# Performance work log

Hardware: AMD Instinct MI355X
Metric: run time of the kernel (lower is better)

Reference implementation:

```python
import jax, jax.numpy as jnp
import numpy as np

B, T, C, H = 4, 1024, 512, 4
D = C // H
N_LAYER, LAYER_ID = 12, 1


def setup_inputs() -> dict:
    key = jax.random.key(0)
    ks = jax.random.split(key, 10)
    w = lambda k, shape: 0.02 * jax.random.normal(k, shape, dtype=jnp.float32)

    r01 = LAYER_ID / (N_LAYER - 1)          # ratio_0_to_1
    r1a0 = 1.0 - LAYER_ID / N_LAYER          # ratio_1_to_almost0
    i = np.arange(C, dtype=np.float32)
    time_decay = (-5.0 + 8.0 * (i / (C - 1)) ** (0.7 + 1.3 * r01)).astype(np.float32)
    xv = i / C
    tm_q = (xv ** r1a0).astype(np.float32)[None, None, :]
    tm_k = (xv ** r1a0).astype(np.float32)[None, None, :]
    tm_v = ((xv ** r1a0) + 0.3 * r01).astype(np.float32)[None, None, :]
    tm_g = (xv ** (0.5 * r1a0)).astype(np.float32)[None, None, :]

    return dict(
        x=jax.random.normal(ks[0], (B, T, C), dtype=jnp.float32),
        ln1_g=jnp.ones((C,), jnp.float32), ln1_b=jnp.zeros((C,), jnp.float32),
        ln2_g=jnp.ones((C,), jnp.float32), ln2_b=jnp.zeros((C,), jnp.float32),
        time_decay=jnp.asarray(time_decay),
        tm_q=jnp.asarray(tm_q), tm_k=jnp.asarray(tm_k),
        tm_v=jnp.asarray(tm_v), tm_g=jnp.asarray(tm_g),
        Wq=w(ks[1], (C, C)), Wk=w(ks[2], (C, C)), Wv=w(ks[3], (C, C)),
        Wg=w(ks[4], (C, C)), Wo=w(ks[5], (C, C)),
        rms_scale=jnp.ones((C,), jnp.float32),
        W1=w(ks[6], (4 * C, C)), W2=w(ks[7], (C, 4 * C)),
    )


def layernorm(x, g, b, eps=1e-5):
    m = x.mean(-1, keepdims=True)
    v = ((x - m) ** 2).mean(-1, keepdims=True)
    return g * (x - m) / jnp.sqrt(v + eps) + b


def rmsnorm(x, scale, eps=1e-8):
    # matches: norm = ||x||_2 / sqrt(dim); out = scale * x / (norm + eps)
    norm = jnp.sqrt(jnp.sum(x * x, axis=-1, keepdims=True)) / (x.shape[-1] ** 0.5)
    return scale * (x / (norm + eps))


def lnssm_scan(q, k, v, lam):
    """Decayed linear-attention scan. q,k,v: [B,T,H,D]; lam: [H,D] (decay over k index).
    Returns S: [B,T,H,D] = q_t^T A_t, Zs: [B,T,H] = q_t . z_t."""
    qT, kT, vT = (jnp.moveaxis(a, 1, 0) for a in (q, k, v))  # [T,B,H,D]
    Bq = q.shape[0]
    A0 = jnp.zeros((Bq, q.shape[2], q.shape[3], q.shape[3]), q.dtype)
    z0 = jnp.zeros((Bq, q.shape[2], q.shape[3]), q.dtype)

    def step(carry, inp):
        A, z = carry
        qt, kt, vt = inp
        A = lam[None, :, :, None] * A + kt[..., None] * vt[..., None, :]  # [B,H,Dk,Dv]
        z = lam[None] * z + kt                                            # [B,H,Dk]
        St = jnp.einsum('bhi,bhij->bhj', qt, A)
        Zt = jnp.einsum('bhi,bhi->bh', qt, z)
        return (A, z), (St, Zt)

    _, (S, Zs) = jax.lax.scan(step, (A0, z0), (qT, kT, vT))
    return jnp.moveaxis(S, 0, 1), jnp.moveaxis(Zs, 0, 1)


def reference(x, ln1_g, ln1_b, ln2_g, ln2_b, time_decay, tm_q, tm_k, tm_v, tm_g,
              Wq, Wk, Wv, Wg, Wo, rms_scale, W1, W2):
    Bx, Tx, Cx = x.shape
    Hh, Dd = H, Cx // H

    # --- TimeMix on ln1(x) ---
    h = layernorm(x, ln1_g, ln1_b)
    xx = jnp.concatenate([jnp.zeros_like(h[:, :1]), h[:, :-1]], axis=1)  # time shift
    xq = h * tm_q + xx * (1 - tm_q)
    xk = h * tm_k + xx * (1 - tm_k)
    xv_ = h * tm_v + xx * (1 - tm_v)
    xg = h * tm_g + xx * (1 - tm_g)
    q = xq @ Wq.T
    k = xk @ Wk.T
    v = xv_ @ Wv.T
    g = jax.nn.sigmoid(xg @ Wg.T)
    q = jnp.exp(rmsnorm(q, rms_scale))
    k = jnp.exp(rmsnorm(k, rms_scale))

    lam = jnp.exp(-jnp.exp(time_decay)).reshape(Hh, Dd)
    qh = q.reshape(Bx, Tx, Hh, Dd)
    kh = k.reshape(Bx, Tx, Hh, Dd)
    vh = v.reshape(Bx, Tx, Hh, Dd)
    S, Zs = lnssm_scan(qh, kh, vh, lam)
    att = (S / Zs[..., None]).reshape(Bx, Tx, Cx)
    att = (g * att) @ Wo.T
    x = x + att

    # --- ChannelMix on ln2(x) ---
    h2 = layernorm(x, ln2_g, ln2_b)
    x = x + jax.nn.gelu(h2 @ W1.T, approximate=False) @ W2.T
    return x
```

## Files before the change

kernel.cpp:

```cpp
#include <hip/hip_runtime.h>
#include <math.h>

#define Bb 4
#define Tt 1024
#define Cc 512
#define Hh 4
#define Dd 128
#define Mrows (Bb*Tt)
#define NC 32
#define CL 32
#define AUGB_CB 18432

typedef unsigned short u16;
typedef __attribute__((ext_vector_type(8))) short bf16x8;
typedef __attribute__((ext_vector_type(4))) float f32x4;

__device__ __forceinline__ u16 f2bf(float f) {
  unsigned u = __float_as_uint(f);
  unsigned r = (u + 0x7fffu + ((u >> 16) & 1u)) >> 16;
  return (u16)r;
}
__device__ __forceinline__ float bf2f(u16 v) {
  return __uint_as_float((unsigned)v << 16);
}
__device__ __forceinline__ unsigned pack2(float a, float b) {
  return (unsigned)f2bf(a) | ((unsigned)f2bf(b) << 16);
}
__device__ __forceinline__ float rms_r(const float* __restrict__ ssqp, int zsel, int row) {
  const float* p = ssqp + (size_t)zsel*4*Mrows + row;
  float s2 = p[0] + p[Mrows] + p[2*Mrows] + p[3*Mrows];
  float norm = sqrtf(s2) * 0.044194173824159216f;
  return 1.f / (norm + 1e-8f);
}

__global__ __launch_bounds__(256) void ln1mix_kernel(const float* __restrict__ x,
    const float* __restrict__ g, const float* __restrict__ bta,
    const float* __restrict__ tmq, const float* __restrict__ tmk,
    const float* __restrict__ tmv, const float* __restrict__ tmg,
    u16* __restrict__ xqb, u16* __restrict__ xkb,
    u16* __restrict__ xvb, u16* __restrict__ xgb)
{
  int m = blockIdx.x, tid = threadIdx.x;
  const float* xr = x + (size_t)m * Cc;
  float v0 = xr[tid], v1 = xr[tid + 256];
  bool has = (m & (Tt-1)) != 0;
  float u0 = 0.f, u1 = 0.f;
  if (has) { u0 = xr[tid - Cc]; u1 = xr[(int)tid + 256 - Cc]; }
  float sa = v0 + v1, qa = v0*v0 + v1*v1;
  float sb = u0 + u1, qb = u0*u0 + u1*u1;
  #pragma unroll
  for (int off = 32; off > 0; off >>= 1) {
    sa += __shfl_down(sa, off, 64); qa += __shfl_down(qa, off, 64);
    sb += __shfl_down(sb, off, 64); qb += __shfl_down(qb, off, 64);
  }
  __shared__ float r4[4][4];
  int w = tid >> 6;
  if ((tid & 63) == 0) { r4[w][0]=sa; r4[w][1]=qa; r4[w][2]=sb; r4[w][3]=qb; }
  __syncthreads();
  float Sa = r4[0][0]+r4[1][0]+r4[2][0]+r4[3][0];
  float Qa = r4[0][1]+r4[1][1]+r4[2][1]+r4[3][1];
  float Sb = r4[0][2]+r4[1][2]+r4[2][2]+r4[3][2];
  float Qb = r4[0][3]+r4[1][3]+r4[2][3]+r4[3][3];
  float ma = Sa*(1.f/Cc), va = Qa*(1.f/Cc) - ma*ma, ia = rsqrtf(va + 1e-5f);
  float mb = Sb*(1.f/Cc), vb = Qb*(1.f/Cc) - mb*mb, ib = rsqrtf(vb + 1e-5f);
  #pragma unroll
  for (int half = 0; half < 2; ++half) {
    int c = tid + half*256;
    float v = half ? v1 : v0, u = half ? u1 : u0;
    float hv = g[c]*(v - ma)*ia + bta[c];
    float pv = has ? (g[c]*(u - mb)*ib + bta[c]) : 0.f;
    size_t off = ((size_t)(c >> 3) * Mrows + m) * 8 + (c & 7);
    float tq = tmq[c], tk = tmk[c], tv = tmv[c], tg = tmg[c];
    xqb[off] = f2bf(hv*tq + pv*(1.f-tq));
    xkb[off] = f2bf(hv*tk + pv*(1.f-tk));
    xvb[off] = f2bf(hv*tv + pv*(1.f-tv));
    xgb[off] = f2bf(hv*tg + pv*(1.f-tg));
  }
}

__global__ __launch_bounds__(256) void ln2b_kernel(const float* __restrict__ x,
    const float* __restrict__ p0, const float* __restrict__ p1,
    const float* __restrict__ g, const float* __restrict__ bta,
    float* __restrict__ x1, u16* __restrict__ out)
{
  int row = blockIdx.x, tid = threadIdx.x;
  size_t r0 = (size_t)row * Cc + tid, r1 = r0 + 256;
  float v0 = x[r0] + p0[r0] + p1[r0];
  float v1 = x[r1] + p0[r1] + p1[r1];
  x1[r0] = v0; x1[r1] = v1;
  float s = v0 + v1, s2 = v0*v0 + v1*v1;
  #pragma unroll
  for (int off = 32; off > 0; off >>= 1) {
    s  += __shfl_down(s,  off, 64);
    s2 += __shfl_down(s2, off, 64);
  }
  __shared__ float rs[4], rq[4];
  int w = tid >> 6;
  if ((tid & 63) == 0) { rs[w] = s; rq[w] = s2; }
  __syncthreads();
  float S  = rs[0]+rs[1]+rs[2]+rs[3];
  float S2 = rq[0]+rq[1]+rq[2]+rq[3];
  float mean = S * (1.0f/Cc);
  float var  = S2 * (1.0f/Cc) - mean*mean;
  float inv = rsqrtf(var + 1e-5f);
  int c0 = tid, c1 = tid + 256;
  float o0 = g[c0] * (v0-mean)*inv + bta[c0];
  float o1 = g[c1] * (v1-mean)*inv + bta[c1];
  out[((size_t)(c0 >> 3) * Mrows + row) * 8 + (c0 & 7)] = f2bf(o0);
  out[((size_t)(c1 >> 3) * Mrows + row) * 8 + (c1 & 7)] = f2bf(o1);
}

__global__ __launch_bounds__(256) void wconv_all_kernel(
    const float* __restrict__ Wq, const float* __restrict__ Wk,
    const float* __restrict__ Wv, const float* __restrict__ Wg,
    const float* __restrict__ Wo, const float* __restrict__ W1,
    const float* __restrict__ W2, u16* __restrict__ out)
{
  int blk = blockIdx.x;
  const float* src; u16* dst; int K, nshift;
  if (blk < 640) {
    int wsel = blk >> 7;
    src = wsel==0?Wq:wsel==1?Wk:wsel==2?Wv:wsel==3?Wg:Wo;
    dst = out + (size_t)wsel*262144; K = 512; nshift = 9; blk &= 127;
  } else if (blk < 1152) {
    src = W1; dst = out + (size_t)5*262144; K = 512; nshift = 11; blk -= 640;
  } else {
    src = W2; dst = out + (size_t)5*262144 + 1048576; K = 2048; nshift = 9; blk -= 1152;
  }
  int i = blk*256 + threadIdx.x;
  int n = i & ((1 << nshift) - 1), kg = i >> nshift;
  const float* p = src + (size_t)n * K + kg * 8;
  float4 a = *(const float4*)p, b = *(const float4*)(p + 4);
  uint4 o;
  o.x = pack2(a.x, a.y); o.y = pack2(a.z, a.w);
  o.z = pack2(b.x, b.y); o.w = pack2(b.z, b.w);
  *(uint4*)(dst + (size_t)i * 8) = o;
}

template<int MR, int NR, int KR>
__device__ __forceinline__ void gemm_core(const u16* __restrict__ A,
    const u16* __restrict__ W, const float* __restrict__ res,
    float* __restrict__ outf, u16* __restrict__ outb, int act,
    int m0, int n0, u16* Asm, u16* Bsm, float* __restrict__ ssq)
{
  const int tid = threadIdx.x, w = tid >> 6, l = tid & 63;
  const int wr = w >> 1, wc = w & 1;
  f32x4 acc[4][4];
  #pragma unroll
  for (int i = 0; i < 4; ++i)
    #pragma unroll
    for (int j = 0; j < 4; ++j) acc[i][j] = (f32x4){0.f,0.f,0.f,0.f};
  const int kgl = l >> 4, rl = l & 15;
  const int q = w * 4;

  #define STAGE(KT, BUF) do {                                               \
    _Pragma("unroll")                                                       \
    for (int ii = 0; ii < 4; ++ii) {                                        \
      int qq = q + ii;                                                      \
      int isB = qq >> 3, idx = qq & 7, kg = idx >> 1, hf = idx & 1;         \
      const u16* src = isB                                                  \
        ? W + ((size_t)((KT)*4 + kg) * NR + n0 + hf*64 + l) * 8             \
        : A + ((size_t)((KT)*4 + kg) * MR + m0 + hf*64 + l) * 8;            \
      u16* dst = (isB ? Bsm : Asm) + (BUF)*4096 + (kg * 128 + hf * 64) * 8; \
      __builtin_amdgcn_global_load_lds(                                     \
          (const __attribute__((address_space(1))) void*)src,               \
          (__attribute__((address_space(3))) void*)dst, 16, 0, 0);          \
    }                                                                       \
  } while (0)

  constexpr int nk = KR >> 5;
  STAGE(0, 0); STAGE(1, 1);
  int cur = 0;
  for (int kt = 0; kt < nk; ++kt) {
    if (kt == nk - 1) asm volatile("s_waitcnt vmcnt(0)" ::: "memory");
    else              asm volatile("s_waitcnt vmcnt(4)" ::: "memory");
    __builtin_amdgcn_s_barrier();
    bf16x8 af[4], bfr[4];
    #pragma unroll
    for (int f = 0; f < 4; ++f)
      af[f] = *(const bf16x8*)&Asm[cur*4096 + (kgl*128 + wr*64 + f*16 + rl) * 8];
    #pragma unroll
    for (int f = 0; f < 4; ++f)
      bfr[f] = *(const bf16x8*)&Bsm[cur*4096 + (kgl*128 + wc*64 + f*16 + rl) * 8];
    if (kt + 2 < nk) {
      int nb = cur + 2; if (nb >= 3) nb -= 3;
      STAGE(kt + 2, nb);
    }
    __builtin_amdgcn_s_setprio(1);
    #pragma unroll
    for (int i = 0; i < 4; ++i)
      #pragma unroll
      for (int j = 0; j < 4; ++j)
        acc[i][j] = __builtin_amdgcn_mfma_f32_16x16x32_bf16(af[i], bfr[j], acc[i][j], 0, 0, 0);
    __builtin_amdgcn_s_setprio(0);
    if (++cur == 3) cur = 0;
  }
  #undef STAGE

  const int rbase = (l >> 4) * 4, cn = l & 15;
  #pragma unroll
  for (int i = 0; i < 4; ++i) {
    #pragma unroll
    for (int j = 0; j < 4; ++j) {
      #pragma unroll
      for (int r = 0; r < 4; ++r) {
        int m = m0 + wr*64 + i*16 + rbase + r;
        int n = n0 + wc*64 + j*16 + cn;
        float vv = acc[i][j][r];
        if (res) vv += res[(size_t)m * NR + n];
        if (act == 1) vv = 0.5f*vv*(1.f + erff(vv * 0.70710678118f));
        else if (act == 2) vv = 1.f/(1.f + expf(-vv));
        if (outb) outb[((size_t)(n >> 3) * MR + m) * 8 + (n & 7)] = f2bf(vv);
        else outf[(size_t)m * NR + n] = vv;
      }
    }
  }

  if (ssq) {
    __syncthreads();
    float* red2 = (float*)Asm;
    #pragma unroll
    for (int i = 0; i < 4; ++i) {
      #pragma unroll
      for (int r = 0; r < 4; ++r) {
        int row_local = wr*64 + i*16 + rbase + r;
        float sq = 0.f;
        #pragma unroll
        for (int j = 0; j < 4; ++j) { float t = acc[i][j][r]; sq += t*t; }
        red2[row_local*32 + wc*16 + cn] = sq;
      }
    }
    __syncthreads();
    if (tid < 128) {
      float ssum = 0.f;
      #pragma unroll
      for (int u2 = 0; u2 < 32; ++u2) ssum += red2[tid*32 + u2];
      ssq[m0 + tid] = ssum;
    }
  }
}

__global__ __launch_bounds__(256) void gemm_qkvg(const u16* __restrict__ xall,
    const u16* __restrict__ Wall, float* __restrict__ outall, float* __restrict__ ssqp)
{
  __shared__ __align__(16) u16 Asm[3*4096];
  __shared__ __align__(16) u16 Bsm[3*4096];
  int z = blockIdx.z;
  const size_t E = (size_t)Mrows * Cc;
  float* ssq = (z < 2) ? ssqp + ((size_t)z*4 + blockIdx.x)*Mrows : nullptr;
  gemm_core<Mrows,512,512>(xall + z*E, Wall + (size_t)z*262144, nullptr,
            outall + z*E, nullptr, z == 3 ? 2 : 0,
            blockIdx.y * 128, blockIdx.x * 128, Asm, Bsm, ssq);
}

__global__ __launch_bounds__(256) void gemm_wo(const u16* __restrict__ A,
    const u16* __restrict__ W, float* __restrict__ pbuf)
{
  __shared__ __align__(16) u16 Asm[3*4096];
  __shared__ __align__(16) u16 Bsm[3*4096];
  int z = blockIdx.z;
  const size_t E = (size_t)Mrows * Cc;
  gemm_core<Mrows,512,256>(A + (size_t)z*32*Mrows*8, W + (size_t)z*32*512*8, nullptr,
            pbuf + z*E, nullptr, 0, blockIdx.y * 128, blockIdx.x * 128, Asm, Bsm, nullptr);
}

__global__ __launch_bounds__(256) void gemm_w1(const u16* __restrict__ A,
    const u16* __restrict__ W, u16* __restrict__ outb)
{
  __shared__ __align__(16) u16 Asm[3*4096];
  __shared__ __align__(16) u16 Bsm[3*4096];
  gemm_core<Mrows,2048,512>(A, W, nullptr, nullptr, outb, 1,
            blockIdx.y * 128, blockIdx.x * 128, Asm, Bsm, nullptr);
}

__global__ __launch_bounds__(256) void gemm_w2(const u16* __restrict__ A,
    const u16* __restrict__ W, float* __restrict__ pbuf)
{
  __shared__ __align__(16) u16 Asm[3*4096];
  __shared__ __align__(16) u16 Bsm[3*4096];
  int z = blockIdx.z;
  const size_t E = (size_t)Mrows * Cc;
  gemm_core<Mrows,512,512>(A + (size_t)z*64*Mrows*8, W + (size_t)z*64*512*8, nullptr,
            pbuf + z*E, nullptr, 0, blockIdx.y * 128, blockIdx.x * 128, Asm, Bsm, nullptr);
}

__global__ __launch_bounds__(256) void reduce4_kernel(const float* __restrict__ x1,
    const float* __restrict__ p, float* __restrict__ out)
{
  const size_t E = (size_t)Mrows * Cc;
  size_t f = ((size_t)blockIdx.x * 256 + threadIdx.x) * 4;
  float4 a = *(const float4*)(x1 + f);
  float4 q0 = *(const float4*)(p + f);
  float4 q1 = *(const float4*)(p + E + f);
  float4 q2 = *(const float4*)(p + 2*E + f);
  float4 q3 = *(const float4*)(p + 3*E + f);
  float4 o;
  o.x = a.x + q0.x + q1.x + q2.x + q3.x;
  o.y = a.y + q0.y + q1.y + q2.y + q3.y;
  o.z = a.z + q0.z + q1.z + q2.z + q3.z;
  o.w = a.w + q0.w + q1.w + q2.w + q3.w;
  *(float4*)(out + f) = o;
}

__global__ __launch_bounds__(256) void chunk_state_kernel(const float* __restrict__ k,
    const float* __restrict__ v, const float* __restrict__ td,
    const float* __restrict__ rsc, const float* __restrict__ ssqp,
    u16* __restrict__ Augl)
{
  __shared__ float k_lds[CL][Dd];
  __shared__ float v_lds[CL][Dd];
  int blk = blockIdx.x; int c = blk & (NC-1); int bh = blk >> 5;
  int b = bh >> 2, h = bh & 3;
  int tid = threadIdx.x;
  size_t base = ((size_t)b*Tt + (size_t)c*CL)*Cc + h*Dd;
  #pragma unroll
  for (int r = 0; r < 4; ++r) {
    int idx4 = r*256 + tid;
    int s = idx4 >> 5; int i4 = (idx4 & 31) << 2;
    float rk = rms_r(ssqp, 1, b*Tt + c*CL + s);
    float4 kr = *(const float4*)&k[base + (size_t)s*Cc + i4];
    k_lds[s][i4+0] = expf(rsc[h*Dd+i4+0] * kr.x * rk);
    k_lds[s][i4+1] = expf(rsc[h*Dd+i4+1] * kr.y * rk);
    k_lds[s][i4+2] = expf(rsc[h*Dd+i4+2] * kr.z * rk);
    k_lds[s][i4+3] = expf(rsc[h*Dd+i4+3] * kr.w * rk);
    *(float4*)&v_lds[s][i4] = *(const float4*)&v[base + (size_t)s*Cc + i4];
  }
  __syncthreads();
  int iq = tid >> 3; int i0 = iq << 2;
  int jg = tid & 7;  int j0 = jg << 4;
  float lam4[4], powv[4], zacc[4];
  #pragma unroll
  for (int ci=0; ci<4; ++ci) {
    lam4[ci] = expf(-expf(td[h*Dd + i0 + ci]));
    powv[ci] = 1.f; zacc[ci] = 0.f;
  }
  float acc[4][16];
  #pragma unroll
  for (int ci=0; ci<4; ++ci)
    #pragma unroll
    for (int jj=0; jj<16; ++jj) acc[ci][jj] = 0.f;

  for (int s = CL-1; s >= 0; --s) {
    float4 k4 = *(const float4*)&k_lds[s][i0];
    float kw0 = powv[0]*k4.x, kw1 = powv[1]*k4.y, kw2 = powv[2]*k4.z, kw3 = powv[3]*k4.w;
    zacc[0]+=kw0; zacc[1]+=kw1; zacc[2]+=kw2; zacc[3]+=kw3;
    #pragma unroll
    for (int q4 = 0; q4 < 4; ++q4) {
      float4 v4 = *(const float4*)&v_lds[s][j0 + q4*4];
      float vv[4] = {v4.x, v4.y, v4.z, v4.w};
      #pragma unroll
      for (int u=0; u<4; ++u) {
        acc[0][q4*4+u] += kw0*vv[u];
        acc[1][q4*4+u] += kw1*vv[u];
        acc[2][q4*4+u] += kw2*vv[u];
        acc[3][q4*4+u] += kw3*vv[u];
      }
    }
    powv[0]*=lam4[0]; powv[1]*=lam4[1]; powv[2]*=lam4[2]; powv[3]*=lam4[3];
  }
  u16* aug = Augl + ((size_t)c*16 + bh)*AUGB_CB;
  const int ig = i0 >> 3, isub = i0 & 7;
  #pragma unroll
  for (int jj=0; jj<16; ++jj) {
    int j = j0 + jj;
    uint2 pk;
    pk.x = pack2(acc[0][jj], acc[1][jj]);
    pk.y = pack2(acc[2][jj], acc[3][jj]);
    *(uint2*)&aug[(size_t)ig*1152 + (size_t)j*8 + isub] = pk;
  }
  if (jg == 0) {
    uint2 pk;
    pk.x = pack2(zacc[0], zacc[1]);
    pk.y = pack2(zacc[2], zacc[3]);
    *(uint2*)&aug[(size_t)ig*1152 + 128*8 + isub] = pk;
  }
}

__global__ __launch_bounds__(256) void combine_kernel(const u16* __restrict__ Augl,
    const float* __restrict__ td, u16* __restrict__ Augb)
{
  int idx = blockIdx.x*256 + threadIdx.x;
  if (idx >= 129*128) return;
  int bh = blockIdx.y; int h = bh & 3;
  int j = idx >> 7, i = idx & 127;
  size_t aoff = (size_t)(i >> 3) * 1152 + (size_t)j * 8 + (i & 7);
  float lamL = expf(-expf(td[h*Dd + i]) * (float)CL);
  const u16* pl = Augl + (size_t)bh*AUGB_CB + aoff;
  u16* pi = Augb + (size_t)bh*AUGB_CB + aoff;
  float prev = 0.f;
  const size_t cstr = (size_t)16*AUGB_CB;
  for (int c = 0; c < NC; ++c) {
    float val = bf2f(pl[c*cstr]);
    pi[c*cstr] = f2bf(prev);
    prev = lamL*prev + val;
  }
}

__global__ __launch_bounds__(256, 2) void scan_mfma_kernel(
    const float* __restrict__ q, const float* __restrict__ k,
    const float* __restrict__ v, const float* __restrict__ td,
    const float* __restrict__ rsc, const float* __restrict__ ssqp,
    const u16* __restrict__ Augb, const float* __restrict__ gmat,
    u16* __restrict__ out)
{
  __shared__ float k_lds[32*192];
  __shared__ u16  qfrag[32*128];
  __shared__ u16  vfrag[4*1152];
  __shared__ float P32[32*33];
  __shared__ u16  pfrag[32*32];
  __shared__ float lam_lds[128];
  __shared__ float zbuf[32];

  const int tid = threadIdx.x;
  const int blk = blockIdx.x; const int c = blk & 31, bh = blk >> 5;
  const int b = bh >> 2, h = bh & 3;
  const int w = tid >> 6, l = tid & 63;
  const int t = (w << 3) + (l >> 3);
  const int is = l & 7;

  if (tid < 128) lam_lds[tid] = expf(-expf(td[h*Dd + tid]));

  const int grow = b*Tt + c*CL + t;
  const size_t rowbase = ((size_t)grow)*Cc + h*Dd + is*16;
  const float rq = rms_r(ssqp, 0, grow);
  const float rk = rms_r(ssqp, 1, grow);

  float qv[16];
  {
    #pragma unroll
    for (int c4 = 0; c4 < 4; ++c4) {
      float4 q4 = *(const float4*)(q + rowbase + c4*4);
      int e0 = c4*4;
      qv[e0+0] = expf(rsc[h*Dd+is*16+e0+0] * q4.x * rq);
      qv[e0+1] = expf(rsc[h*Dd+is*16+e0+1] * q4.y * rq);
      qv[e0+2] = expf(rsc[h*Dd+is*16+e0+2] * q4.z * rq);
      qv[e0+3] = expf(rsc[h*Dd+is*16+e0+3] * q4.w * rq);
    }
    float lt = (float)(t + 1);
    u16 qt[16];
    #pragma unroll
    for (int e = 0; e < 16; ++e) {
      float el2 = -expf(td[h*Dd + is*16 + e]) * 1.4426950408889634f;
      qt[e] = f2bf(qv[e] * exp2f(el2 * lt));
    }
    #pragma unroll
    for (int hf = 0; hf < 2; ++hf) {
      int k8 = is*2 + hf;
      uint4 pk;
      pk.x = (unsigned)qt[hf*8+0] | ((unsigned)qt[hf*8+1]<<16);
      pk.y = (unsigned)qt[hf*8+2] | ((unsigned)qt[hf*8+3]<<16);
      pk.z = (unsigned)qt[hf*8+4] | ((unsigned)qt[hf*8+5]<<16);
      pk.w = (unsigned)qt[hf*8+6] | ((unsigned)qt[hf*8+7]<<16);
      *(uint4*)&qfrag[t*128 + ((k8 ^ (t&7))<<3)] = pk;
    }
  }
  #pragma unroll
  for (int c4 = 0; c4 < 4; ++c4) {
    float4 k4 = *(const float4*)(k + rowbase + c4*4);
    int e0 = is*16 + c4*4;
    k_lds[t*192 + is*24 + c4*4+0] = expf(rsc[h*Dd+e0+0] * k4.x * rk);
    k_lds[t*192 + is*24 + c4*4+1] = expf(rsc[h*Dd+e0+1] * k4.y * rk);
    k_lds[t*192 + is*24 + c4*4+2] = expf(rsc[h*Dd+e0+2] * k4.z * rk);
    k_lds[t*192 + is*24 + c4*4+3] = expf(rsc[h*Dd+e0+3] * k4.w * rk);
  }
  #pragma unroll
  for (int c4 = 0; c4 < 4; ++c4) {
    float4 v4 = *(const float4*)(v + rowbase + c4*4);
    int j0 = is*16 + c4*4;
    vfrag[(t>>3)*1152 + (j0+0)*8 + (t&7)] = f2bf(v4.x);
    vfrag[(t>>3)*1152 + (j0+1)*8 + (t&7)] = f2bf(v4.y);
    vfrag[(t>>3)*1152 + (j0+2)*8 + (t&7)] = f2bf(v4.z);
    vfrag[(t>>3)*1152 + (j0+3)*8 + (t&7)] = f2bf(v4.w);
  }
  if (tid < 32) vfrag[(tid>>3)*1152 + 128*8 + (tid&7)] = 0x3F80;
  if (tid < 240) {
    #pragma unroll
    for (int u = 0; u < 2; ++u) {
      int e = tid*2 + u;
      int ig = e / 120, rem = e % 120;
      vfrag[ig*1152 + (129 + rem/8)*8 + (rem&7)] = 0;
    }
  }
  __syncthreads();

  {
    float lamr[16], wrun[16];
    #pragma unroll
    for (int e4 = 0; e4 < 4; ++e4) {
      float4 l4 = *(const float4*)&lam_lds[is*16 + e4*4];
      lamr[e4*4+0]=l4.x; lamr[e4*4+1]=l4.y; lamr[e4*4+2]=l4.z; lamr[e4*4+3]=l4.w;
    }
    #pragma unroll
    for (int e = 0; e < 16; ++e) wrun[e] = 1.f;
    const int smax = (w << 3) + 7;
    for (int s = smax; s >= 0; --s) {
      float dot = 0.f;
      #pragma unroll
      for (int c4 = 0; c4 < 4; ++c4) {
        float4 k4 = *(const float4*)&k_lds[s*192 + is*24 + c4*4];
        dot = fmaf(qv[c4*4+0], k4.x*wrun[c4*4+0], dot);
        dot = fmaf(qv[c4*4+1], k4.y*wrun[c4*4+1], dot);
        dot = fmaf(qv[c4*4+2], k4.z*wrun[c4*4+2], dot);
        dot = fmaf(qv[c4*4+3], k4.w*wrun[c4*4+3], dot);
      }
      dot += __shfl_xor(dot, 1);
      dot += __shfl_xor(dot, 2);
      dot += __shfl_xor(dot, 4);
      bool act = (s <= t);
      if (act && is == 0) P32[t*33 + s] = dot;
      if (act) {
        #pragma unroll
        for (int e = 0; e < 16; ++e) wrun[e] *= lamr[e];
      }
    }
  }
  __syncthreads();
  {
    int tt = tid >> 3, s0 = (tid & 7) * 4;
    #pragma unroll
    for (int ss = 0; ss < 4; ++ss) {
      int s = s0 + ss;
      float val = (s <= tt) ? P32[tt*33 + s] : 0.f;
      pfrag[tt*32 + (((s>>3) ^ (tt&3))<<3) + (s&7)] = f2bf(val);
    }
  }
  __syncthreads();

  const int tau = w >> 1;
  const int jt0 = (w & 1) ? 5 : 0;
  const int njt = (w & 1) ? 4 : 5;
  const int rl = l & 15, kg = l >> 4;
  const int trow = tau*16 + rl;
  const u16* augb_base = Augb + ((size_t)c*16 + bh)*AUGB_CB;

  bf16x8 aq[4];
  #pragma unroll
  for (int kk = 0; kk < 4; ++kk)
    aq[kk] = *(const bf16x8*)&qfrag[trow*128 + ((((kk<<2)+kg) ^ (trow&7))<<3)];
  bf16x8 ap = *(const bf16x8*)&pfrag[trow*32 + ((kg ^ (trow&3))<<3)];

  f32x4 acc[5];
  #pragma unroll
  for (int u = 0; u < 5; ++u) acc[u] = (f32x4){0.f,0.f,0.f,0.f};

  #pragma unroll
  for (int u = 0; u < 5; ++u) {
    if (u < njt) {
      int jt = jt0 + u;
      #pragma unroll
      for (int kk = 0; kk < 4; ++kk) {
        bf16x8 bfr = *(const bf16x8*)&augb_base[(size_t)(((kk<<2)+kg)*1152 + (jt*16 + rl)*8)];
        acc[u] = __builtin_amdgcn_mfma_f32_16x16x32_bf16(aq[kk], bfr, acc[u], 0, 0, 0);
      }
      bf16x8 bv = *(const bf16x8*)&vfrag[kg*1152 + (jt*16 + rl)*8];
      acc[u] = __builtin_amdgcn_mfma_f32_16x16x32_bf16(ap, bv, acc[u], 0, 0, 0);
    }
  }
  if ((w & 1) && rl == 0) {
    #pragma unroll
    for (int r = 0; r < 4; ++r) zbuf[tau*16 + kg*4 + r] = acc[3][r];
  }
  __syncthreads();

  const int nout = (w & 1) ? 3 : 5;
  #pragma unroll
  for (int u = 0; u < 5; ++u) {
    if (u < nout) {
      int jt = jt0 + u;
      int cc = h*Dd + jt*16 + rl;
      #pragma unroll
      for (int r = 0; r < 4; ++r) {
        int tr = tau*16 + kg*4 + r;
        int m = b*Tt + c*CL + tr;
        float zv = zbuf[tr];
        float gv = gmat[(size_t)m*Cc + cc];
        out[((size_t)(cc >> 3) * Mrows + m) * 8 + (cc & 7)] = f2bf(gv * acc[u][r] / zv);
      }
    }
  }
}

extern "C" void kernel_launch(void* const* d_in, const int* in_sizes, int n_in,
                              void* d_out, int out_size, void* d_ws, size_t ws_size,
                              hipStream_t stream) {
  const float* x    = (const float*)d_in[0];
  const float* ln1g = (const float*)d_in[1];
  const float* ln1b = (const float*)d_in[2];
  const float* ln2g = (const float*)d_in[3];
  const float* ln2b = (const float*)d_in[4];
  const float* td   = (const float*)d_in[5];
  const float* tmq  = (const float*)d_in[6];
  const float* tmk  = (const float*)d_in[7];
  const float* tmv  = (const float*)d_in[8];
  const float* tmg  = (const float*)d_in[9];
  const float* Wq   = (const float*)d_in[10];
  const float* Wk   = (const float*)d_in[11];
  const float* Wv   = (const float*)d_in[12];
  const float* Wg   = (const float*)d_in[13];
  const float* Wo   = (const float*)d_in[14];
  const float* rsc  = (const float*)d_in[15];
  const float* W1   = (const float*)d_in[16];
  const float* W2   = (const float*)d_in[17];
  float* ws = (float*)d_ws;
  const size_t E = (size_t)Mrows*Cc;
  float* s0 = ws;
  float* s1 = ws + E;
  float* s2 = ws + 2*E;
  float* s3 = ws + 3*E;
  float* x1 = ws + 4*E;
  u16* xqb = (u16*)(ws + 5*E);
  u16* xkb = xqb + E;
  u16* xvb = xkb + E;
  u16* xgb = xvb + E;
  u16* wreg = (u16*)(ws + 7*E);
  u16* Wqb = wreg;
  u16* Wob = wreg + 4*262144;
  u16* W1b = wreg + 5*262144;
  u16* W2b = W1b + 1048576;
  u16* Augl = W2b + 1048576;
  u16* Augb = Augl + (size_t)NC*16*AUGB_CB;
  float* ssqp = (float*)(Augb + (size_t)NC*16*AUGB_CB);
  u16* midb  = Augl;
  u16* gattb = xqb;
  u16* h2b   = xkb;

  wconv_all_kernel<<<1664,256,0,stream>>>(Wq, Wk, Wv, Wg, Wo, W1, W2, Wqb);
  ln1mix_kernel<<<Mrows,256,0,stream>>>(x, ln1g, ln1b, tmq,tmk,tmv,tmg,
                                        xqb,xkb,xvb,xgb);
  gemm_qkvg<<<dim3(4,32,4),256,0,stream>>>(xqb, Wqb, s0, ssqp);
  chunk_state_kernel<<<16*NC,256,0,stream>>>(s1, s2, td, rsc, ssqp, Augl);
  combine_kernel<<<dim3(65,16),256,0,stream>>>(Augl, td, Augb);
  scan_mfma_kernel<<<16*NC,256,0,stream>>>(s0, s1, s2, td, rsc, ssqp, Augb, s3, gattb);
  gemm_wo<<<dim3(4,32,2),256,0,stream>>>(gattb, Wob, s2);
  ln2b_kernel<<<Mrows,256,0,stream>>>(x, s2, s3, ln2g, ln2b, x1, h2b);
  gemm_w1<<<dim3(16,32),256,0,stream>>>(h2b, W1b, midb);
  gemm_w2<<<dim3(4,32,4),256,0,stream>>>(midb, W2b, s0);
  reduce4_kernel<<<2048,256,0,stream>>>(x1, s0, (float*)d_out);
}
```

Baseline: 168.9 us.

## Shrink GEMM tiles to 64x64, cut split-K, and merge weight conversion into prep

Every GEMM moves from 128x128 tiles to 64x64 tiles with 32x32 per-wave subtiles, which multiplies the block count to fill more CUs. Split-K is removed from the Wo GEMM and halved in the W2 GEMM, so the ln2 and final reduction kernels read fewer partial buffers. The RMS sum-of-squares partials grow from 4 to 8 per row to match the narrower N tiles. The weight bf16 conversion is merged into the layernorm/mix kernel to save a launch. The trade-off is lower data reuse per tile, meaning more global and LDS traffic per FLOP, plus a larger ssqp buffer that must still fit the workspace.

```diff
diff --git a/kernel.cpp b/kernel.cpp
--- a/kernel.cpp
+++ b/kernel.cpp
@@ -27,20 +27,49 @@
   return (unsigned)f2bf(a) | ((unsigned)f2bf(b) << 16);
 }
 __device__ __forceinline__ float rms_r(const float* __restrict__ ssqp, int zsel, int row) {
-  const float* p = ssqp + (size_t)zsel*4*Mrows + row;
-  float s2 = p[0] + p[Mrows] + p[2*Mrows] + p[3*Mrows];
+  const float* p = ssqp + (size_t)zsel*8*Mrows + row;
+  float s2 = 0.f;
+  #pragma unroll
+  for (int u = 0; u < 8; ++u) s2 += p[(size_t)u*Mrows];
   float norm = sqrtf(s2) * 0.044194173824159216f;
   return 1.f / (norm + 1e-8f);
 }
 
-__global__ __launch_bounds__(256) void ln1mix_kernel(const float* __restrict__ x,
+__global__ __launch_bounds__(256) void prep_kernel(const float* __restrict__ x,
     const float* __restrict__ g, const float* __restrict__ bta,
     const float* __restrict__ tmq, const float* __restrict__ tmk,
     const float* __restrict__ tmv, const float* __restrict__ tmg,
     u16* __restrict__ xqb, u16* __restrict__ xkb,
-    u16* __restrict__ xvb, u16* __restrict__ xgb)
-{
-  int m = blockIdx.x, tid = threadIdx.x;
+    u16* __restrict__ xvb, u16* __restrict__ xgb,
+    const float* __restrict__ Wq, const float* __restrict__ Wk,
+    const float* __restrict__ Wv, const float* __restrict__ Wg,
+    const float* __restrict__ Wo, const float* __restrict__ W1,
+    const float* __restrict__ W2, u16* __restrict__ wout)
+{
+  int tid = threadIdx.x;
+  if (blockIdx.x >= 4096) {
+    int blk = blockIdx.x - 4096;
+    const float* src; u16* dst; int K, nshift;
+    if (blk < 640) {
+      int wsel = blk >> 7;
+      src = wsel==0?Wq:wsel==1?Wk:wsel==2?Wv:wsel==3?Wg:Wo;
+      dst = wout + (size_t)wsel*262144; K = 512; nshift = 9; blk &= 127;
+    } else if (blk < 1152) {
+      src = W1; dst = wout + (size_t)5*262144; K = 512; nshift = 11; blk -= 640;
+    } else {
+      src = W2; dst = wout + (size_t)5*262144 + 1048576; K = 2048; nshift = 9; blk -= 1152;
+    }
+    int i = blk*256 + tid;
+    int n = i & ((1 << nshift) - 1), kg = i >> nshift;
+    const float* p = src + (size_t)n * K + kg * 8;
+    float4 a = *(const float4*)p, b = *(const float4*)(p + 4);
+    uint4 o;
+    o.x = pack2(a.x, a.y); o.y = pack2(a.z, a.w);
+    o.z = pack2(b.x, b.y); o.w = pack2(b.z, b.w);
+    *(uint4*)(dst + (size_t)i * 8) = o;
+    return;
+  }
+  int m = blockIdx.x;
   const float* xr = x + (size_t)m * Cc;
   float v0 = xr[tid], v1 = xr[tid + 256];
   bool has = (m & (Tt-1)) != 0;
@@ -79,14 +108,14 @@
 }
 
 __global__ __launch_bounds__(256) void ln2b_kernel(const float* __restrict__ x,
-    const float* __restrict__ p0, const float* __restrict__ p1,
+    const float* __restrict__ p0,
     const float* __restrict__ g, const float* __restrict__ bta,
     float* __restrict__ x1, u16* __restrict__ out)
 {
   int row = blockIdx.x, tid = threadIdx.x;
   size_t r0 = (size_t)row * Cc + tid, r1 = r0 + 256;
-  float v0 = x[r0] + p0[r0] + p1[r0];
-  float v1 = x[r1] + p0[r1] + p1[r1];
+  float v0 = x[r0] + p0[r0];
+  float v1 = x[r1] + p0[r1];
   x1[r0] = v0; x1[r1] = v1;
   float s = v0 + v1, s2 = v0*v0 + v1*v1;
   #pragma unroll
@@ -110,58 +139,31 @@
   out[((size_t)(c1 >> 3) * Mrows + row) * 8 + (c1 & 7)] = f2bf(o1);
 }
 
-__global__ __launch_bounds__(256) void wconv_all_kernel(
-    const float* __restrict__ Wq, const float* __restrict__ Wk,
-    const float* __restrict__ Wv, const float* __restrict__ Wg,
-    const float* __restrict__ Wo, const float* __restrict__ W1,
-    const float* __restrict__ W2, u16* __restrict__ out)
-{
-  int blk = blockIdx.x;
-  const float* src; u16* dst; int K, nshift;
-  if (blk < 640) {
-    int wsel = blk >> 7;
-    src = wsel==0?Wq:wsel==1?Wk:wsel==2?Wv:wsel==3?Wg:Wo;
-    dst = out + (size_t)wsel*262144; K = 512; nshift = 9; blk &= 127;
-  } else if (blk < 1152) {
-    src = W1; dst = out + (size_t)5*262144; K = 512; nshift = 11; blk -= 640;
-  } else {
-    src = W2; dst = out + (size_t)5*262144 + 1048576; K = 2048; nshift = 9; blk -= 1152;
-  }
-  int i = blk*256 + threadIdx.x;
-  int n = i & ((1 << nshift) - 1), kg = i >> nshift;
-  const float* p = src + (size_t)n * K + kg * 8;
-  float4 a = *(const float4*)p, b = *(const float4*)(p + 4);
-  uint4 o;
-  o.x = pack2(a.x, a.y); o.y = pack2(a.z, a.w);
-  o.z = pack2(b.x, b.y); o.w = pack2(b.z, b.w);
-  *(uint4*)(dst + (size_t)i * 8) = o;
-}
-
 template<int MR, int NR, int KR>
-__device__ __forceinline__ void gemm_core(const u16* __restrict__ A,
+__device__ __forceinline__ void gemm_core64(const u16* __restrict__ A,
     const u16* __restrict__ W, const float* __restrict__ res,
     float* __restrict__ outf, u16* __restrict__ outb, int act,
     int m0, int n0, u16* Asm, u16* Bsm, float* __restrict__ ssq)
 {
   const int tid = threadIdx.x, w = tid >> 6, l = tid & 63;
   const int wr = w >> 1, wc = w & 1;
-  f32x4 acc[4][4];
-  #pragma unroll
-  for (int i = 0; i < 4; ++i)
-    #pragma unroll
-    for (int j = 0; j < 4; ++j) acc[i][j] = (f32x4){0.f,0.f,0.f,0.f};
+  f32x4 acc[2][2];
+  #pragma unroll
+  for (int i = 0; i < 2; ++i)
+    #pragma unroll
+    for (int j = 0; j < 2; ++j) acc[i][j] = (f32x4){0.f,0.f,0.f,0.f};
   const int kgl = l >> 4, rl = l & 15;
-  const int q = w * 4;
+  const int q = w * 2;
 
   #define STAGE(KT, BUF) do {                                               \
     _Pragma("unroll")                                                       \
-    for (int ii = 0; ii < 4; ++ii) {                                        \
+    for (int ii = 0; ii < 2; ++ii) {                                        \
       int qq = q + ii;                                                      \
-      int isB = qq >> 3, idx = qq & 7, kg = idx >> 1, hf = idx & 1;         \
+      int isB = qq >> 2, kg = qq & 3;                                       \
       const u16* src = isB                                                  \
-        ? W + ((size_t)((KT)*4 + kg) * NR + n0 + hf*64 + l) * 8             \
-        : A + ((size_t)((KT)*4 + kg) * MR + m0 + hf*64 + l) * 8;            \
-      u16* dst = (isB ? Bsm : Asm) + (BUF)*4096 + (kg * 128 + hf * 64) * 8; \
+        ? W + ((size_t)((KT)*4 + kg) * NR + n0 + l) * 8                     \
+        : A + ((size_t)((KT)*4 + kg) * MR + m0 + l) * 8;                    \
+      u16* dst = (isB ? Bsm : Asm) + (BUF)*2048 + kg * 64 * 8;              \
       __builtin_amdgcn_global_load_lds(                                     \
           (const __attribute__((address_space(1))) void*)src,               \
           (__attribute__((address_space(3))) void*)dst, 16, 0, 0);          \
@@ -173,24 +175,24 @@
   int cur = 0;
   for (int kt = 0; kt < nk; ++kt) {
     if (kt == nk - 1) asm volatile("s_waitcnt vmcnt(0)" ::: "memory");
-    else              asm volatile("s_waitcnt vmcnt(4)" ::: "memory");
+    else              asm volatile("s_waitcnt vmcnt(2)" ::: "memory");
     __builtin_amdgcn_s_barrier();
-    bf16x8 af[4], bfr[4];
-    #pragma unroll
-    for (int f = 0; f < 4; ++f)
-      af[f] = *(const bf16x8*)&Asm[cur*4096 + (kgl*128 + wr*64 + f*16 + rl) * 8];
-    #pragma unroll
-    for (int f = 0; f < 4; ++f)
-      bfr[f] = *(const bf16x8*)&Bsm[cur*4096 + (kgl*128 + wc*64 + f*16 + rl) * 8];
+    bf16x8 af[2], bfr[2];
+    #pragma unroll
+    for (int f = 0; f < 2; ++f)
+      af[f] = *(const bf16x8*)&Asm[cur*2048 + (kgl*64 + wr*32 + f*16 + rl) * 8];
+    #pragma unroll
+    for (int f = 0; f < 2; ++f)
+      bfr[f] = *(const bf16x8*)&Bsm[cur*2048 + (kgl*64 + wc*32 + f*16 + rl) * 8];
     if (kt + 2 < nk) {
       int nb = cur + 2; if (nb >= 3) nb -= 3;
       STAGE(kt + 2, nb);
     }
     __builtin_amdgcn_s_setprio(1);
     #pragma unroll
-    for (int i = 0; i < 4; ++i)
-      #pragma unroll
-      for (int j = 0; j < 4; ++j)
+    for (int i = 0; i < 2; ++i)
+      #pragma unroll
+      for (int j = 0; j < 2; ++j)
         acc[i][j] = __builtin_amdgcn_mfma_f32_16x16x32_bf16(af[i], bfr[j], acc[i][j], 0, 0, 0);
     __builtin_amdgcn_s_setprio(0);
     if (++cur == 3) cur = 0;
@@ -199,13 +201,13 @@
 
   const int rbase = (l >> 4) * 4, cn = l & 15;
   #pragma unroll
-  for (int i = 0; i < 4; ++i) {
-    #pragma unroll
-    for (int j = 0; j < 4; ++j) {
+  for (int i = 0; i < 2; ++i) {
+    #pragma unroll
+    for (int j = 0; j < 2; ++j) {
       #pragma unroll
       for (int r = 0; r < 4; ++r) {
-        int m = m0 + wr*64 + i*16 + rbase + r;
-        int n = n0 + wc*64 + j*16 + cn;
+        int m = m0 + wr*32 + i*16 + rbase + r;
+        int n = n0 + wc*32 + j*16 + cn;
         float vv = acc[i][j][r];
         if (res) vv += res[(size_t)m * NR + n];
         if (act == 1) vv = 0.5f*vv*(1.f + erff(vv * 0.70710678118f));
@@ -220,18 +222,18 @@
     __syncthreads();
     float* red2 = (float*)Asm;
     #pragma unroll
-    for (int i = 0; i < 4; ++i) {
+    for (int i = 0; i < 2; ++i) {
       #pragma unroll
       for (int r = 0; r < 4; ++r) {
-        int row_local = wr*64 + i*16 + rbase + r;
+        int row_local = wr*32 + i*16 + rbase + r;
         float sq = 0.f;
         #pragma unroll
-        for (int j = 0; j < 4; ++j) { float t = acc[i][j][r]; sq += t*t; }
+        for (int j = 0; j < 2; ++j) { float t = acc[i][j][r]; sq += t*t; }
         red2[row_local*32 + wc*16 + cn] = sq;
       }
     }
     __syncthreads();
-    if (tid < 128) {
+    if (tid < 64) {
       float ssum = 0.f;
       #pragma unroll
       for (int u2 = 0; u2 < 32; ++u2) ssum += red2[tid*32 + u2];
@@ -243,48 +245,46 @@
 __global__ __launch_bounds__(256) void gemm_qkvg(const u16* __restrict__ xall,
     const u16* __restrict__ Wall, float* __restrict__ outall, float* __restrict__ ssqp)
 {
-  __shared__ __align__(16) u16 Asm[3*4096];
-  __shared__ __align__(16) u16 Bsm[3*4096];
+  __shared__ __align__(16) u16 Asm[3*2048];
+  __shared__ __align__(16) u16 Bsm[3*2048];
   int z = blockIdx.z;
   const size_t E = (size_t)Mrows * Cc;
-  float* ssq = (z < 2) ? ssqp + ((size_t)z*4 + blockIdx.x)*Mrows : nullptr;
-  gemm_core<Mrows,512,512>(xall + z*E, Wall + (size_t)z*262144, nullptr,
+  float* ssq = (z < 2) ? ssqp + ((size_t)z*8 + blockIdx.x)*Mrows : nullptr;
+  gemm_core64<Mrows,512,512>(xall + z*E, Wall + (size_t)z*262144, nullptr,
             outall + z*E, nullptr, z == 3 ? 2 : 0,
-            blockIdx.y * 128, blockIdx.x * 128, Asm, Bsm, ssq);
+            blockIdx.y * 64, blockIdx.x * 64, Asm, Bsm, ssq);
 }
 
 __global__ __launch_bounds__(256) void gemm_wo(const u16* __restrict__ A,
+    const u16* __restrict__ W, float* __restrict__ outf)
+{
+  __shared__ __align__(16) u16 Asm[3*2048];
+  __shared__ __align__(16) u16 Bsm[3*2048];
+  gemm_core64<Mrows,512,512>(A, W, nullptr, outf, nullptr, 0,
+            blockIdx.y * 64, blockIdx.x * 64, Asm, Bsm, nullptr);
+}
+
+__global__ __launch_bounds__(256) void gemm_w1(const u16* __restrict__ A,
+    const u16* __restrict__ W, u16* __restrict__ outb)
+{
+  __shared__ __align__(16) u16 Asm[3*2048];
+  __shared__ __align__(16) u16 Bsm[3*2048];
+  gemm_core64<Mrows,2048,512>(A, W, nullptr, nullptr, outb, 1,
+            blockIdx.y * 64, blockIdx.x * 64, Asm, Bsm, nullptr);
+}
+
+__global__ __launch_bounds__(256) void gemm_w2(const u16* __restrict__ A,
     const u16* __restrict__ W, float* __restrict__ pbuf)
 {
-  __shared__ __align__(16) u16 Asm[3*4096];
-  __shared__ __align__(16) u16 Bsm[3*4096];
+  __shared__ __align__(16) u16 Asm[3*2048];
+  __shared__ __align__(16) u16 Bsm[3*2048];
   int z = blockIdx.z;
   const size_t E = (size_t)Mrows * Cc;
-  gemm_core<Mrows,512,256>(A + (size_t)z*32*Mrows*8, W + (size_t)z*32*512*8, nullptr,
-            pbuf + z*E, nullptr, 0, blockIdx.y * 128, blockIdx.x * 128, Asm, Bsm, nullptr);
-}
-
-__global__ __launch_bounds__(256) void gemm_w1(const u16* __restrict__ A,
-    const u16* __restrict__ W, u16* __restrict__ outb)
-{
-  __shared__ __align__(16) u16 Asm[3*4096];
-  __shared__ __align__(16) u16 Bsm[3*4096];
-  gemm_core<Mrows,2048,512>(A, W, nullptr, nullptr, outb, 1,
-            blockIdx.y * 128, blockIdx.x * 128, Asm, Bsm, nullptr);
-}
-
-__global__ __launch_bounds__(256) void gemm_w2(const u16* __restrict__ A,
-    const u16* __restrict__ W, float* __restrict__ pbuf)
-{
-  __shared__ __align__(16) u16 Asm[3*4096];
-  __shared__ __align__(16) u16 Bsm[3*4096];
-  int z = blockIdx.z;
-  const size_t E = (size_t)Mrows * Cc;
-  gemm_core<Mrows,512,512>(A + (size_t)z*64*Mrows*8, W + (size_t)z*64*512*8, nullptr,
-            pbuf + z*E, nullptr, 0, blockIdx.y * 128, blockIdx.x * 128, Asm, Bsm, nullptr);
-}
-
-__global__ __launch_bounds__(256) void reduce4_kernel(const float* __restrict__ x1,
+  gemm_core64<Mrows,512,1024>(A + (size_t)z*128*Mrows*8, W + (size_t)z*128*512*8, nullptr,
+            pbuf + z*E, nullptr, 0, blockIdx.y * 64, blockIdx.x * 64, Asm, Bsm, nullptr);
+}
+
+__global__ __launch_bounds__(256) void reduce2_kernel(const float* __restrict__ x1,
     const float* __restrict__ p, float* __restrict__ out)
 {
   const size_t E = (size_t)Mrows * Cc;
@@ -292,13 +292,11 @@
   float4 a = *(const float4*)(x1 + f);
   float4 q0 = *(const float4*)(p + f);
   float4 q1 = *(const float4*)(p + E + f);
-  float4 q2 = *(const float4*)(p + 2*E + f);
-  float4 q3 = *(const float4*)(p + 3*E + f);
   float4 o;
-  o.x = a.x + q0.x + q1.x + q2.x + q3.x;
-  o.y = a.y + q0.y + q1.y + q2.y + q3.y;
-  o.z = a.z + q0.z + q1.z + q2.z + q3.z;
-  o.w = a.w + q0.w + q1.w + q2.w + q3.w;
+  o.x = a.x + q0.x + q1.x;
+  o.y = a.y + q0.y + q1.y;
+  o.z = a.z + q0.z + q1.z;
+  o.w = a.w + q0.w + q1.w;
   *(float4*)(out + f) = o;
 }
 
@@ -624,16 +622,16 @@
   u16* gattb = xqb;
   u16* h2b   = xkb;
 
-  wconv_all_kernel<<<1664,256,0,stream>>>(Wq, Wk, Wv, Wg, Wo, W1, W2, Wqb);
-  ln1mix_kernel<<<Mrows,256,0,stream>>>(x, ln1g, ln1b, tmq,tmk,tmv,tmg,
-                                        xqb,xkb,xvb,xgb);
-  gemm_qkvg<<<dim3(4,32,4),256,0,stream>>>(xqb, Wqb, s0, ssqp);
+  prep_kernel<<<5760,256,0,stream>>>(x, ln1g, ln1b, tmq,tmk,tmv,tmg,
+                                     xqb,xkb,xvb,xgb,
+                                     Wq, Wk, Wv, Wg, Wo, W1, W2, Wqb);
+  gemm_qkvg<<<dim3(8,64,4),256,0,stream>>>(xqb, Wqb, s0, ssqp);
   chunk_state_kernel<<<16*NC,256,0,stream>>>(s1, s2, td, rsc, ssqp, Augl);
   combine_kernel<<<dim3(65,16),256,0,stream>>>(Augl, td, Augb);
   scan_mfma_kernel<<<16*NC,256,0,stream>>>(s0, s1, s2, td, rsc, ssqp, Augb, s3, gattb);
-  gemm_wo<<<dim3(4,32,2),256,0,stream>>>(gattb, Wob, s2);
-  ln2b_kernel<<<Mrows,256,0,stream>>>(x, s2, s3, ln2g, ln2b, x1, h2b);
-  gemm_w1<<<dim3(16,32),256,0,stream>>>(h2b, W1b, midb);
-  gemm_w2<<<dim3(4,32,4),256,0,stream>>>(midb, W2b, s0);
-  reduce4_kernel<<<2048,256,0,stream>>>(x1, s0, (float*)d_out);
-}
+  gemm_wo<<<dim3(8,64),256,0,stream>>>(gattb, Wob, s2);
+  ln2b_kernel<<<Mrows,256,0,stream>>>(x, s2, ln2g, ln2b, x1, h2b);
+  gemm_w1<<<dim3(32,64),256,0,stream>>>(h2b, W1b, midb);
+  gemm_w2<<<dim3(8,64,2),256,0,stream>>>(midb, W2b, s0);
+  reduce2_kernel<<<2048,256,0,stream>>>(x1, s0, (float*)d_out);
+}
```

Measured after the change: 173.3 us. 1.03x slower.
